# Performance work log

Measured on AMD Instinct MI355X. Metric: run time of the kernel, lower is better.

## Reference

```python
import jax, jax.numpy as jnp
import numpy as np

N, E, D, R, L, B, K = 10000, 160000, 256, 237, 6, 128, 33
EPS = 1e-6


def setup_inputs() -> dict:
    key = jax.random.key(0)
    ks = jax.random.split(key, 8)
    x = jax.random.uniform(ks[0], (N, D), dtype=jnp.float32)
    edge_index = jax.random.randint(ks[1], (2, E), 0, N)
    edge_type = jax.random.randint(ks[2], (E,), 0, R)
    batch = jax.random.randint(ks[3], (B, K, 3), 0, R)
    rel_embs = jax.random.normal(ks[4], (L, R, D), dtype=jnp.float32) * 0.02
    Ws = jax.random.normal(ks[5], (L, 13 * D, D), dtype=jnp.float32) * 0.02
    bs = jnp.zeros((L, D), dtype=jnp.float32)
    ln_scale = jnp.ones((L, D), dtype=jnp.float32)
    ln_bias = jnp.zeros((L, D), dtype=jnp.float32)
    relation_emb = jax.random.normal(ks[6], (R, D), dtype=jnp.float32) * 0.02
    return dict(x=x, rel_embs=rel_embs, Ws=Ws, bs=bs, ln_scale=ln_scale,
                ln_bias=ln_bias, relation_emb=relation_emb,
                edge_index=edge_index, edge_type=edge_type, batch=batch)


def _layer_norm(h, g, b, eps=1e-5):
    mu = jnp.mean(h, axis=-1, keepdims=True)
    var = jnp.var(h, axis=-1, keepdims=True)
    return (h - mu) * jax.lax.rsqrt(var + eps) * g + b


def _rgcn_conv(x, edge_index, edge_type, rel, W, b, g, be):
    # DistMult message + self-loop boundary, PNA aggregation, linear+LN+ReLU.
    n, d = x.shape
    src, dst = edge_index[0], edge_index[1]
    msg = x[src] * rel[edge_type]                       # [E, D]
    msg = jnp.concatenate([msg, x], axis=0)             # self-loop messages
    seg = jnp.concatenate([dst, jnp.arange(n)], axis=0)
    deg = jax.ops.segment_sum(jnp.ones((msg.shape[0],), jnp.float32), seg, n)  # >= 1
    inv_deg = 1.0 / deg[:, None]
    mean = jax.ops.segment_sum(msg, seg, n) * inv_deg
    sq_mean = jax.ops.segment_sum(msg * msg, seg, n) * inv_deg
    mx = jax.ops.segment_max(msg, seg, n)
    mn = jax.ops.segment_min(msg, seg, n)
    std = jnp.sqrt(jnp.clip(sq_mean - mean * mean, EPS))
    feats = jnp.concatenate([mean, mx, mn, std], axis=-1)          # [N, 4D]
    scale = jnp.log(deg)
    scale = scale / jnp.mean(scale)
    scales = jnp.stack([jnp.ones_like(scale), scale,
                        1.0 / jnp.clip(scale, 1e-2)], axis=-1)      # [N, 3]
    agg = (feats[:, :, None] * scales[:, None, :]).reshape(n, 12 * d)
    h = jnp.concatenate([agg, x], axis=-1) @ W + b                  # [N, D]
    return jax.nn.relu(_layer_norm(h, g, be))


def reference(x, rel_embs, Ws, bs, ln_scale, ln_bias, relation_emb,
              edge_index, edge_type, batch):
    for i in range(L):  # loop over layers (structurally distinct params)
        x = _rgcn_conv(x, edge_index, edge_type, rel_embs[i], Ws[i],
                       bs[i], ln_scale[i], ln_bias[i]) + x  # short_cut
    s = x[batch[:, :, 0]]                 # [B, K, D]
    r = relation_emb[batch[:, :, 1]]      # [B, K, D]
    t = x[batch[:, :, 2]]                 # [B, K, D]
    return jnp.sum(s * r * t, axis=-1)    # [B, K] DistMult scores
```

## Files before the change

kernel.cpp:

```cpp
#include <hip/hip_runtime.h>
#include <math.h>

typedef __attribute__((ext_vector_type(8))) _Float16 half8;
typedef __attribute__((ext_vector_type(4))) _Float16 half4;
typedef __attribute__((ext_vector_type(4))) float    floatx4;
typedef __attribute__((ext_vector_type(2))) float    float2v;

#define N_NODES 10000
#define M_PAD   10112
#define MTILES  79
#define E_EDGES 160000
#define DIM     256
#define R_REL   237
#define L_LAYERS 6
#define B_BATCH 128
#define K_BATCH 33
#define K13     3328
#define WL_STRIDE 851968
#define EPS_STD 1e-6f
#define EPS_LN  1e-5f

__device__ __forceinline__ void gload16(const void* g, void* lds) {
    __builtin_amdgcn_global_load_lds(
        (const __attribute__((address_space(1))) unsigned int*)g,
        (__attribute__((address_space(3))) unsigned int*)lds, 16, 0, 0);
}

__device__ __forceinline__ unsigned pkmax16(unsigned a, unsigned b) {
    unsigned r;
    asm("v_pk_max_f16 %0, %1, %2" : "=v"(r) : "v"(a), "v"(b));
    return r;
}
__device__ __forceinline__ unsigned pkmin16(unsigned a, unsigned b) {
    unsigned r;
    asm("v_pk_min_f16 %0, %1, %2" : "=v"(r) : "v"(a), "v"(b));
    return r;
}
typedef union { half8 h; unsigned u[4]; } h8u;

__global__ void hist_kernel(const int* __restrict__ dst, int* __restrict__ deg) {
    int e = blockIdx.x * blockDim.x + threadIdx.x;
    if (e < E_EDGES) atomicAdd(&deg[dst[e]], 1);
}

__global__ void scan_kernel(const int* __restrict__ deg_in, int* __restrict__ offs,
                            int* __restrict__ cursor, float* __restrict__ sum_log) {
    __shared__ int   part[1024];
    __shared__ float slog[1024];
    int t = threadIdx.x;
    const int CH = 10;
    int base = t * CH;
    int lsum = 0; float ls = 0.f;
    for (int j = 0; j < CH; j++) {
        int i = base + j;
        if (i < N_NODES) { int d = deg_in[i]; lsum += d; ls += logf((float)(d + 1)); }
    }
    part[t] = lsum; slog[t] = ls;
    __syncthreads();
    for (int off = 1; off < 1024; off <<= 1) {
        int v = (t >= off) ? part[t - off] : 0;
        __syncthreads();
        part[t] += v;
        __syncthreads();
    }
    int run = part[t] - lsum;
    for (int j = 0; j < CH; j++) {
        int i = base + j;
        if (i < N_NODES) { offs[i] = run; cursor[i] = run; run += deg_in[i]; }
    }
    __syncthreads();
    for (int off = 512; off > 0; off >>= 1) {
        if (t < off) slog[t] += slog[t + off];
        __syncthreads();
    }
    if (t == 0) sum_log[0] = slog[0];
}

__global__ void fill_kernel(const int* __restrict__ src, const int* __restrict__ dst,
                            const int* __restrict__ et, int* __restrict__ cursor,
                            int2* __restrict__ csr) {
    int e = blockIdx.x * blockDim.x + threadIdx.x;
    if (e < E_EDGES) {
        int d = dst[e];
        int p = atomicAdd(&cursor[d], 1);
        csr[p] = make_int2(src[e], et[e]);
    }
}

__global__ void scales_kernel(const int* __restrict__ deg_in, const float* __restrict__ sum_log,
                              float* __restrict__ s1, float* __restrict__ s2) {
    int i = blockIdx.x * blockDim.x + threadIdx.x;
    if (i < N_NODES) {
        float mean = sum_log[0] * (1.0f / (float)N_NODES);
        float sc = logf((float)(deg_in[i] + 1)) / mean;
        s1[i] = sc;
        s2[i] = 1.0f / fmaxf(sc, 0.01f);
    }
}

__global__ void wt_kernel(const float* __restrict__ Ws, _Float16* __restrict__ Wt) {
    __shared__ float tile[64][65];
    int b = blockIdx.x;
    int l = b / 208;
    int r = b - l * 208;
    int spanel = (r < 192) ? 1 : 0;
    int sidx = 0, kt, nt;
    if (spanel) { sidx = r >> 6; int r2 = r & 63; kt = r2 >> 2; nt = r2 & 3; }
    else        { int r2 = r - 192; kt = r2 >> 2; nt = r2 & 3; }
    int k0 = kt * 64, n0 = nt * 64;
    int tid = threadIdx.x;
    int rr = tid >> 4;
    int cc = tid & 15;
    const float* srcL = Ws + (size_t)l * K13 * 256;
    #pragma unroll
    for (int p = 0; p < 4; p++) {
        int krow = p * 16 + rr;
        int korig = spanel ? (k0 + krow) * 3 + sidx : 3072 + k0 + krow;
        float4 v = *(const float4*)(srcL + (size_t)korig * 256 + n0 + cc * 4);
        tile[krow][cc * 4 + 0] = v.x;
        tile[krow][cc * 4 + 1] = v.y;
        tile[krow][cc * 4 + 2] = v.z;
        tile[krow][cc * 4 + 3] = v.w;
    }
    __syncthreads();
    _Float16* outL = Wt + (size_t)l * WL_STRIDE;
    #pragma unroll
    for (int p = 0; p < 4; p++) {
        int nrow = p * 16 + rr;
        int kk = cc * 4;
        half4 hv = { (_Float16)tile[kk + 0][nrow], (_Float16)tile[kk + 1][nrow],
                     (_Float16)tile[kk + 2][nrow], (_Float16)tile[kk + 3][nrow] };
        size_t oo = spanel ? ((size_t)sidx * 262144 + (size_t)(n0 + nrow) * 1024 + k0 + kk)
                           : ((size_t)786432 + (size_t)(n0 + nrow) * 256 + k0 + kk);
        *(half4*)(outL + oo) = hv;
    }
}

__global__ void cvt_kernel(const float* __restrict__ in, _Float16* __restrict__ outp, int n) {
    int i = blockIdx.x * 256 + threadIdx.x;
    if (i < n) outp[i] = (_Float16)in[i];
}

__global__ void agg_kernel(const float* __restrict__ x, const _Float16* __restrict__ xh,
                           const _Float16* __restrict__ relh,
                           const int* __restrict__ offs, const int* __restrict__ deg_in,
                           const int2* __restrict__ csr, _Float16* __restrict__ feats) {
    int wid  = threadIdx.x >> 6;
    int lane = threadIdx.x & 63;
    int node = blockIdx.x * 4 + wid;
    if (node >= N_NODES) return;
    int half = lane >> 5;
    int sub  = lane & 31;
    int off = offs[node];
    int dc  = deg_in[node];
    int npairs = dc >> 1;
    const half8* xh8 = (const half8*)xh;
    const half8* rh8 = (const half8*)relh;

    float2v s2[4], q2[4];
    unsigned mxu[4], mnu[4];
    #pragma unroll
    for (int i = 0; i < 4; i++) {
        s2[i] = (float2v){0.f, 0.f};
        q2[i] = (float2v){0.f, 0.f};
        mxu[i] = 0xFC00FC00u;
        mnu[i] = 0x7C007C00u;
    }

    const int2* ep = csr + off + half;
    for (int p = 0; p < npairs; p++) {
        int2 se = ep[2 * p];
        half8 xv = xh8[(size_t)se.x * 32 + sub];
        half8 rv = rh8[(size_t)se.y * 32 + sub];
        half8 mv = xv * rv;
        h8u mu; mu.h = mv;
        #pragma unroll
        for (int i = 0; i < 4; i++) {
            mxu[i] = pkmax16(mxu[i], mu.u[i]);
            mnu[i] = pkmin16(mnu[i], mu.u[i]);
            float2v mf = { (float)mv[2*i], (float)mv[2*i+1] };
            s2[i] += mf;
            q2[i] += mf * mf;
        }
    }
    if (dc & 1) {
        int2 se = csr[off + dc - 1];
        half8 xv = xh8[(size_t)se.x * 32 + sub];
        half8 rv = rh8[(size_t)se.y * 32 + sub];
        half8 mv = xv * rv;
        h8u mu; mu.h = mv;
        #pragma unroll
        for (int i = 0; i < 4; i++) {
            mxu[i] = pkmax16(mxu[i], mu.u[i]);
            mnu[i] = pkmin16(mnu[i], mu.u[i]);
            float2v mf = { (float)mv[2*i], (float)mv[2*i+1] };
            s2[i] += 0.5f * mf;
            q2[i] += (0.5f * mf) * mf;
        }
    }
    float s_[8], q_[8], mx_[8], mn_[8];
    #pragma unroll
    for (int i = 0; i < 4; i++) {
        mxu[i] = pkmax16(mxu[i], (unsigned)__shfl_xor((int)mxu[i], 32));
        mnu[i] = pkmin16(mnu[i], (unsigned)__shfl_xor((int)mnu[i], 32));
        h8u tx; tx.u[0] = mxu[i]; h8u tn; tn.u[0] = mnu[i];
        mx_[2*i]   = (float)tx.h[0]; mx_[2*i+1] = (float)tx.h[1];
        mn_[2*i]   = (float)tn.h[0]; mn_[2*i+1] = (float)tn.h[1];
        s_[2*i]   = s2[i].x + __shfl_xor(s2[i].x, 32);
        s_[2*i+1] = s2[i].y + __shfl_xor(s2[i].y, 32);
        q_[2*i]   = q2[i].x + __shfl_xor(q2[i].x, 32);
        q_[2*i+1] = q2[i].y + __shfl_xor(q2[i].y, 32);
    }
    const float4* xrow = (const float4*)(x + (size_t)node * 256);
    float4 xa = xrow[sub * 2], xb = xrow[sub * 2 + 1];
    float xs[8] = {xa.x, xa.y, xa.z, xa.w, xb.x, xb.y, xb.z, xb.w};
    #pragma unroll
    for (int i = 0; i < 8; i++) {
        s_[i] += xs[i]; q_[i] += xs[i] * xs[i];
        mx_[i] = fmaxf(mx_[i], xs[i]);
        mn_[i] = fminf(mn_[i], xs[i]);
    }
    float inv = 1.0f / (float)(dc + 1);
    half8 hm, hx, hn, hs;
    #pragma unroll
    for (int i = 0; i < 8; i++) {
        float mean = s_[i] * inv;
        float sd = sqrtf(fmaxf(q_[i] * inv - mean * mean, EPS_STD));
        hm[i] = (_Float16)mean; hx[i] = (_Float16)mx_[i];
        hn[i] = (_Float16)mn_[i]; hs[i] = (_Float16)sd;
    }
    half8* fout = (half8*)(feats + (size_t)node * 1024);
    if (half == 0) {
        fout[0 * 32 + sub] = hm;
        fout[1 * 32 + sub] = hx;
    } else {
        fout[2 * 32 + sub] = hn;
        fout[3 * 32 + sub] = hs;
    }
}

__launch_bounds__(256, 3)
__global__ void gemm_kernel(const _Float16* __restrict__ feats, const _Float16* __restrict__ xh,
                            const _Float16* __restrict__ Wl, _Float16* __restrict__ hbuf) {
    __shared__ _Float16 sA[3][128 * 32];
    __shared__ _Float16 sB[3][128 * 32];

    int xcd = blockIdx.x & 7, loc = blockIdx.x >> 3;
    int lin = xcd * MTILES + loc;
    int sidx = lin & 3;
    int nh   = (lin >> 2) & 1;
    int m    = lin >> 3;
    const int i0 = m * 128;
    const int n0 = nh * 128;
    const int NS  = (sidx == 3) ? 8 : 32;
    const int nit = (NS - 2) / 3;

    const int tid   = threadIdx.x;
    const int lane  = tid & 63;
    const int w     = tid >> 6;
    const int wr    = w >> 1;
    const int wc    = w & 1;
    const int row_l = lane & 15;
    const int kq    = lane >> 4;

    int a_off[4], b_off[4];
    #pragma unroll
    for (int rf = 0; rf < 4; rf++) {
        int r = wr * 64 + rf * 16 + row_l;
        a_off[rf] = r * 32 + ((kq ^ ((r >> 1) & 3)) & 3) * 8;
    }
    #pragma unroll
    for (int cf = 0; cf < 4; cf++) {
        int n_ = wc * 64 + cf * 16 + row_l;
        b_off[cf] = n_ * 32 + ((kq ^ ((n_ >> 1) & 3)) & 3) * 8;
    }

    const char* a_src[2];
    const char* b_src[2];
    #pragma unroll
    for (int j = 0; j < 2; j++) {
        int rloc = j * 64 + w * 16 + (lane >> 2);
        int c = (lane & 3) ^ ((rloc >> 1) & 3);
        if (sidx < 3) {
            a_src[j] = (const char*)(feats + (size_t)(i0 + rloc) * 1024 + c * 8);
            b_src[j] = (const char*)(Wl + (size_t)sidx * 262144 + (size_t)(n0 + rloc) * 1024 + c * 8);
        } else {
            a_src[j] = (const char*)(xh + (size_t)(i0 + rloc) * 256 + c * 8);
            b_src[j] = (const char*)(Wl + 786432 + (size_t)(n0 + rloc) * 256 + c * 8);
        }
    }

    floatx4 acc[4][4];
    #pragma unroll
    for (int rf = 0; rf < 4; rf++)
        #pragma unroll
        for (int cf = 0; cf < 4; cf++)
            acc[rf][cf] = (floatx4){0.f, 0.f, 0.f, 0.f};

#define STAGE(BUF, S) do {                                                    \
    size_t koff_ = (size_t)(S) * 64;                                          \
    gload16(a_src[0] + koff_, (char*)(&sA[BUF][0]) + (0 * 64 + w * 16) * 64); \
    gload16(a_src[1] + koff_, (char*)(&sA[BUF][0]) + (1 * 64 + w * 16) * 64); \
    gload16(b_src[0] + koff_, (char*)(&sB[BUF][0]) + (0 * 64 + w * 16) * 64); \
    gload16(b_src[1] + koff_, (char*)(&sB[BUF][0]) + (1 * 64 + w * 16) * 64); \
} while (0)

#define COMPUTE(CB) do {                                                      \
    half8 af[4], bf[4];                                                       \
    _Pragma("unroll")                                                         \
    for (int rf = 0; rf < 4; rf++) af[rf] = *(const half8*)(&sA[CB][a_off[rf]]); \
    _Pragma("unroll")                                                         \
    for (int cf = 0; cf < 4; cf++) bf[cf] = *(const half8*)(&sB[CB][b_off[cf]]); \
    _Pragma("unroll")                                                         \
    for (int rf = 0; rf < 4; rf++)                                            \
        _Pragma("unroll")                                                     \
        for (int cf = 0; cf < 4; cf++)                                        \
            acc[rf][cf] = __builtin_amdgcn_mfma_f32_16x16x32_f16(af[rf], bf[cf], acc[rf][cf], 0, 0, 0); \
} while (0)

#define STEP(S, CB, NB) do {                                                  \
    asm volatile("s_waitcnt vmcnt(4)" ::: "memory");                          \
    __builtin_amdgcn_s_barrier();                                             \
    STAGE(NB, (S) + 2);                                                       \
    COMPUTE(CB);                                                              \
} while (0)

    STAGE(0, 0);
    STAGE(1, 1);

    for (int it = 0; it < nit; ++it) {
        int s = it * 3;
        STEP(s + 0, 0, 2);
        STEP(s + 1, 1, 0);
        STEP(s + 2, 2, 1);
    }
    asm volatile("s_waitcnt vmcnt(4)" ::: "memory");
    __builtin_amdgcn_s_barrier();
    COMPUTE(0);
    asm volatile("s_waitcnt vmcnt(0)" ::: "memory");
    __builtin_amdgcn_s_barrier();
    COMPUTE(1);

#undef STAGE
#undef COMPUTE
#undef STEP

    _Float16* outb = hbuf + (size_t)sidx * M_PAD * 256;
    #pragma unroll
    for (int rf = 0; rf < 4; rf++) {
        #pragma unroll
        for (int j = 0; j < 4; j++) {
            int grow = i0 + wr * 64 + rf * 16 + kq * 4 + j;
            _Float16* orow = outb + (size_t)grow * 256 + n0 + wc * 64;
            #pragma unroll
            for (int cf = 0; cf < 4; cf++)
                orow[cf * 16 + row_l] = (_Float16)acc[rf][cf][j];
        }
    }
}

__global__ void ln_kernel(const _Float16* __restrict__ hbuf, const float* __restrict__ xin,
                          const float* __restrict__ s1a, const float* __restrict__ s2a,
                          const float* __restrict__ bvec, const float* __restrict__ gvec,
                          const float* __restrict__ evec, float* __restrict__ xout,
                          _Float16* __restrict__ xhout) {
    int wid = threadIdx.x >> 6, lane = threadIdx.x & 63;
    int row = blockIdx.x * 4 + wid;
    if (row >= N_NODES) return;
    const half4* p0 = (const half4*)(hbuf + (size_t)row * 256);
    const half4* p1 = (const half4*)(hbuf + (size_t)M_PAD * 256     + (size_t)row * 256);
    const half4* p2 = (const half4*)(hbuf + (size_t)M_PAD * 256 * 2 + (size_t)row * 256);
    const half4* p3 = (const half4*)(hbuf + (size_t)M_PAD * 256 * 3 + (size_t)row * 256);
    half4 h0 = p0[lane], h1 = p1[lane], h2 = p2[lane], h3 = p3[lane];
    float s1v = s1a[row], s2v = s2a[row];
    float4 bv = ((const float4*)bvec)[lane];
    float4 hv;
    hv.x = (float)h0.x + s1v * (float)h1.x + s2v * (float)h2.x + (float)h3.x + bv.x;
    hv.y = (float)h0.y + s1v * (float)h1.y + s2v * (float)h2.y + (float)h3.y + bv.y;
    hv.z = (float)h0.z + s1v * (float)h1.z + s2v * (float)h2.z + (float)h3.z + bv.z;
    hv.w = (float)h0.w + s1v * (float)h1.w + s2v * (float)h2.w + (float)h3.w + bv.w;
    float s = hv.x + hv.y + hv.z + hv.w;
    float qsq = hv.x*hv.x + hv.y*hv.y + hv.z*hv.z + hv.w*hv.w;
    #pragma unroll
    for (int off = 1; off < 64; off <<= 1) {
        s   += __shfl_xor(s, off);
        qsq += __shfl_xor(qsq, off);
    }
    float mu  = s * (1.0f / 256.0f);
    float var = qsq * (1.0f / 256.0f) - mu * mu;
    float rs  = rsqrtf(var + EPS_LN);
    float4 g = ((const float4*)gvec)[lane];
    float4 e = ((const float4*)evec)[lane];
    float4 xv = ((const float4*)(xin + (size_t)row * 256))[lane];
    float4 o;
    o.x = fmaxf((hv.x - mu) * rs * g.x + e.x, 0.f) + xv.x;
    o.y = fmaxf((hv.y - mu) * rs * g.y + e.y, 0.f) + xv.y;
    o.z = fmaxf((hv.z - mu) * rs * g.z + e.z, 0.f) + xv.z;
    o.w = fmaxf((hv.w - mu) * rs * g.w + e.w, 0.f) + xv.w;
    ((float4*)(xout + (size_t)row * 256))[lane] = o;
    half4 oh = { (_Float16)o.x, (_Float16)o.y, (_Float16)o.z, (_Float16)o.w };
    ((half4*)(xhout + (size_t)row * 256))[lane] = oh;
}

__global__ void score_kernel(const float* __restrict__ x, const float* __restrict__ remb,
                             const int* __restrict__ batch, float* __restrict__ out) {
    int wid = threadIdx.x >> 6, lane = threadIdx.x & 63;
    int g = blockIdx.x * 4 + wid;
    if (g >= B_BATCH * K_BATCH) return;
    int si = batch[g * 3 + 0], ri = batch[g * 3 + 1], ti = batch[g * 3 + 2];
    const float4* xs = (const float4*)(x + (size_t)si * 256);
    const float4* xr = (const float4*)(remb + (size_t)ri * 256);
    const float4* xt = (const float4*)(x + (size_t)ti * 256);
    float4 a = xs[lane], r = xr[lane], t = xt[lane];
    float p = a.x*r.x*t.x + a.y*r.y*t.y + a.z*r.z*t.z + a.w*r.w*t.w;
    #pragma unroll
    for (int off = 1; off < 64; off <<= 1) p += __shfl_xor(p, off);
    if (lane == 0) out[g] = p;
}

extern "C" void kernel_launch(void* const* d_in, const int* in_sizes, int n_in,
                              void* d_out, int out_size, void* d_ws, size_t ws_size,
                              hipStream_t stream) {
    const float* x_in     = (const float*)d_in[0];
    const float* rel_embs = (const float*)d_in[1];
    const float* Ws       = (const float*)d_in[2];
    const float* bs       = (const float*)d_in[3];
    const float* ln_s     = (const float*)d_in[4];
    const float* ln_b     = (const float*)d_in[5];
    const float* remb     = (const float*)d_in[6];
    const int*   eidx     = (const int*)d_in[7];
    const int*   etype    = (const int*)d_in[8];
    const int*   batch    = (const int*)d_in[9];
    float* out = (float*)d_out;

    char* wp = (char*)d_ws;
    size_t o = 0;
    auto alloc = [&](size_t bytes) { void* p = wp + o; o += (bytes + 255) & ~255ull; return p; };
    int*      deg_in  = (int*)     alloc((size_t)N_NODES * 4);
    int*      offs    = (int*)     alloc((size_t)N_NODES * 4);
    int*      cursor  = (int*)     alloc((size_t)N_NODES * 4);
    float*    s1      = (float*)   alloc((size_t)M_PAD * 4);
    float*    s2      = (float*)   alloc((size_t)M_PAD * 4);
    float*    sum_log = (float*)   alloc(256);
    int2*     csr     = (int2*)    alloc((size_t)E_EDGES * 8);
    _Float16* feats   = (_Float16*)alloc((size_t)M_PAD * 1024 * 2);
    _Float16* Wt      = (_Float16*)alloc((size_t)L_LAYERS * WL_STRIDE * 2);
    _Float16* hbuf    = (_Float16*)alloc((size_t)4 * M_PAD * 256 * 2);
    float*    xb0     = (float*)   alloc((size_t)M_PAD * 256 * 4);
    float*    xb1     = (float*)   alloc((size_t)M_PAD * 256 * 4);
    _Float16* xh0     = (_Float16*)alloc((size_t)M_PAD * 256 * 2);
    _Float16* xh1     = (_Float16*)alloc((size_t)M_PAD * 256 * 2);
    _Float16* relh    = (_Float16*)alloc((size_t)L_LAYERS * R_REL * 256 * 2);

    const int* src  = eidx;
    const int* dstp = eidx + E_EDGES;

    hipMemsetAsync(deg_in, 0, (size_t)N_NODES * 4, stream);
    hist_kernel<<<(E_EDGES + 255) / 256, 256, 0, stream>>>(dstp, deg_in);
    scan_kernel<<<1, 1024, 0, stream>>>(deg_in, offs, cursor, sum_log);
    fill_kernel<<<(E_EDGES + 255) / 256, 256, 0, stream>>>(src, dstp, etype, cursor, csr);
    scales_kernel<<<(N_NODES + 255) / 256, 256, 0, stream>>>(deg_in, sum_log, s1, s2);
    {
        wt_kernel<<<L_LAYERS * 208, 256, 0, stream>>>(Ws, Wt);
        const int RT = L_LAYERS * R_REL * 256;
        cvt_kernel<<<(RT + 255) / 256, 256, 0, stream>>>(rel_embs, relh, RT);
        const int XT = N_NODES * 256;
        cvt_kernel<<<(XT + 255) / 256, 256, 0, stream>>>(x_in, xh0, XT);
    }
    hipMemcpyAsync(xb0, x_in, (size_t)N_NODES * 256 * 4, hipMemcpyDeviceToDevice, stream);

    float* xc = xb0; float* xn = xb1;
    _Float16* xhc = xh0; _Float16* xhn = xh1;
    for (int l = 0; l < L_LAYERS; l++) {
        agg_kernel<<<(N_NODES + 3) / 4, 256, 0, stream>>>(
            xc, xhc, relh + (size_t)l * R_REL * 256,
            offs, deg_in, csr, feats);
        gemm_kernel<<<632, 256, 0, stream>>>(
            feats, xhc, Wt + (size_t)l * WL_STRIDE, hbuf);
        ln_kernel<<<(N_NODES + 3) / 4, 256, 0, stream>>>(
            hbuf, xc, s1, s2, bs + (size_t)l * 256, ln_s + (size_t)l * 256,
            ln_b + (size_t)l * 256, xn, xhn);
        float* t = xc; xc = xn; xn = t;
        _Float16* th = xhc; xhc = xhn; xhn = th;
    }
    score_kernel<<<(B_BATCH * K_BATCH + 3) / 4, 256, 0, stream>>>(xc, remb, batch, out);
}
```

Baseline: 417.8 us.

## Split each node's edge aggregation across two waves and fuse x initialization

The aggregation kernel now assigns two wavefronts per node, each handling half of the incoming edges. Partial sum, sum-of-squares, max and min results are combined through shared memory after a block barrier. This doubles the number of waves in flight to hide gather latency, at the cost of an extra barrier and LDS traffic. The x fp32 copy and fp16 conversion are also merged into a single vectorized init kernel, replacing a memcpy plus a scalar convert kernel.

```diff
diff --git a/kernel.cpp b/kernel.cpp
--- a/kernel.cpp
+++ b/kernel.cpp
@@ -141,19 +141,37 @@
     if (i < n) outp[i] = (_Float16)in[i];
 }
 
+__global__ void initx_kernel(const float* __restrict__ xin, float* __restrict__ xb,
+                             _Float16* __restrict__ xhout) {
+    int i = blockIdx.x * 256 + threadIdx.x;
+    const int N4 = N_NODES * 64;
+    if (i < N4) {
+        float4 v = ((const float4*)xin)[i];
+        ((float4*)xb)[i] = v;
+        half4 h = { (_Float16)v.x, (_Float16)v.y, (_Float16)v.z, (_Float16)v.w };
+        ((half4*)xhout)[i] = h;
+    }
+}
+
 __global__ void agg_kernel(const float* __restrict__ x, const _Float16* __restrict__ xh,
                            const _Float16* __restrict__ relh,
                            const int* __restrict__ offs, const int* __restrict__ deg_in,
                            const int2* __restrict__ csr, _Float16* __restrict__ feats) {
-    int wid  = threadIdx.x >> 6;
+    __shared__ float part[2][1024];
+    int w    = threadIdx.x >> 6;
     int lane = threadIdx.x & 63;
-    int node = blockIdx.x * 4 + wid;
-    if (node >= N_NODES) return;
+    int nl   = w >> 1;
+    int widx = w & 1;
+    int node = blockIdx.x * 2 + nl;
     int half = lane >> 5;
     int sub  = lane & 31;
     int off = offs[node];
     int dc  = deg_in[node];
-    int npairs = dc >> 1;
+    int c1 = dc >> 1;
+    int c0 = dc - c1;
+    int myoff = off + (widx ? c0 : 0);
+    int myc   = widx ? c1 : c0;
+    int npairs = myc >> 1;
     const half8* xh8 = (const half8*)xh;
     const half8* rh8 = (const half8*)relh;
 
@@ -167,7 +185,7 @@
         mnu[i] = 0x7C007C00u;
     }
 
-    const int2* ep = csr + off + half;
+    const int2* ep = csr + myoff + half;
     for (int p = 0; p < npairs; p++) {
         int2 se = ep[2 * p];
         half8 xv = xh8[(size_t)se.x * 32 + sub];
@@ -183,8 +201,8 @@
             q2[i] += mf * mf;
         }
     }
-    if (dc & 1) {
-        int2 se = csr[off + dc - 1];
+    if (myc & 1) {
+        int2 se = csr[myoff + myc - 1];
         half8 xv = xh8[(size_t)se.x * 32 + sub];
         half8 rv = rh8[(size_t)se.y * 32 + sub];
         half8 mv = xv * rv;
@@ -210,6 +228,42 @@
         s_[2*i+1] = s2[i].y + __shfl_xor(s2[i].y, 32);
         q_[2*i]   = q2[i].x + __shfl_xor(q2[i].x, 32);
         q_[2*i+1] = q2[i].y + __shfl_xor(q2[i].y, 32);
+    }
+    if (widx == 1) {
+        if (half == 0) {
+            *(float4*)&part[nl][0 * 256 + sub * 8]     = (float4){s_[0], s_[1], s_[2], s_[3]};
+            *(float4*)&part[nl][0 * 256 + sub * 8 + 4] = (float4){s_[4], s_[5], s_[6], s_[7]};
+            *(float4*)&part[nl][2 * 256 + sub * 8]     = (float4){mx_[0], mx_[1], mx_[2], mx_[3]};
+            *(float4*)&part[nl][2 * 256 + sub * 8 + 4] = (float4){mx_[4], mx_[5], mx_[6], mx_[7]};
+        } else {
+            *(float4*)&part[nl][1 * 256 + sub * 8]     = (float4){q_[0], q_[1], q_[2], q_[3]};
+            *(float4*)&part[nl][1 * 256 + sub * 8 + 4] = (float4){q_[4], q_[5], q_[6], q_[7]};
+            *(float4*)&part[nl][3 * 256 + sub * 8]     = (float4){mn_[0], mn_[1], mn_[2], mn_[3]};
+            *(float4*)&part[nl][3 * 256 + sub * 8 + 4] = (float4){mn_[4], mn_[5], mn_[6], mn_[7]};
+        }
+    }
+    __syncthreads();
+    if (widx == 1) return;
+
+    {
+        float4 sa = *(const float4*)&part[nl][0 * 256 + sub * 8];
+        float4 sb = *(const float4*)&part[nl][0 * 256 + sub * 8 + 4];
+        float4 qa = *(const float4*)&part[nl][1 * 256 + sub * 8];
+        float4 qb = *(const float4*)&part[nl][1 * 256 + sub * 8 + 4];
+        float4 xa_ = *(const float4*)&part[nl][2 * 256 + sub * 8];
+        float4 xb_ = *(const float4*)&part[nl][2 * 256 + sub * 8 + 4];
+        float4 na = *(const float4*)&part[nl][3 * 256 + sub * 8];
+        float4 nb = *(const float4*)&part[nl][3 * 256 + sub * 8 + 4];
+        float sv[8] = {sa.x, sa.y, sa.z, sa.w, sb.x, sb.y, sb.z, sb.w};
+        float qv[8] = {qa.x, qa.y, qa.z, qa.w, qb.x, qb.y, qb.z, qb.w};
+        float xv_[8] = {xa_.x, xa_.y, xa_.z, xa_.w, xb_.x, xb_.y, xb_.z, xb_.w};
+        float nv[8] = {na.x, na.y, na.z, na.w, nb.x, nb.y, nb.z, nb.w};
+        #pragma unroll
+        for (int i = 0; i < 8; i++) {
+            s_[i] += sv[i]; q_[i] += qv[i];
+            mx_[i] = fmaxf(mx_[i], xv_[i]);
+            mn_[i] = fminf(mn_[i], nv[i]);
+        }
     }
     const float4* xrow = (const float4*)(x + (size_t)node * 256);
     float4 xa = xrow[sub * 2], xb = xrow[sub * 2 + 1];
@@ -464,15 +518,14 @@
         wt_kernel<<<L_LAYERS * 208, 256, 0, stream>>>(Ws, Wt);
         const int RT = L_LAYERS * R_REL * 256;
         cvt_kernel<<<(RT + 255) / 256, 256, 0, stream>>>(rel_embs, relh, RT);
-        const int XT = N_NODES * 256;
-        cvt_kernel<<<(XT + 255) / 256, 256, 0, stream>>>(x_in, xh0, XT);
-    }
-    hipMemcpyAsync(xb0, x_in, (size_t)N_NODES * 256 * 4, hipMemcpyDeviceToDevice, stream);
+        const int X4 = N_NODES * 64;
+        initx_kernel<<<(X4 + 255) / 256, 256, 0, stream>>>(x_in, xb0, xh0);
+    }
 
     float* xc = xb0; float* xn = xb1;
     _Float16* xhc = xh0; _Float16* xhn = xh1;
     for (int l = 0; l < L_LAYERS; l++) {
-        agg_kernel<<<(N_NODES + 3) / 4, 256, 0, stream>>>(
+        agg_kernel<<<N_NODES / 2, 256, 0, stream>>>(
             xc, xhc, relh + (size_t)l * R_REL * 256,
             offs, deg_in, csr, feats);
         gemm_kernel<<<632, 256, 0, stream>>>(
```

New measurement: 419.6 us. Within noise of the previous version (+0.4%).
